# Kernel tuning notes

Hardware: AMD Instinct MI355X
Metric: run time of the kernel (lower is better)

Reference implementation:

```python
import jax, jax.numpy as jnp
import numpy as np

D_MODEL, D_STATE, D_CONV, D_INNER, DT_RANK = 1024, 16, 4, 2048, 64
B_SZ, L = 4, 2048

def setup_inputs() -> dict:
    key = jax.random.key(0)
    ks = jax.random.split(key, 7)
    return {
        "hidden_states": jax.random.normal(ks[0], (B_SZ, L, D_MODEL), jnp.float32),
        "in_proj_w": jax.random.normal(ks[1], (2 * D_INNER, D_MODEL), jnp.float32) * (D_MODEL ** -0.5),
        "conv_w": jax.random.normal(ks[2], (D_INNER, 1, D_CONV), jnp.float32) * 0.5,
        "conv_b": jax.random.normal(ks[3], (D_INNER,), jnp.float32) * 0.1,
        "x_proj_w": jax.random.normal(ks[4], (DT_RANK + 2 * D_STATE, D_INNER), jnp.float32) * (D_INNER ** -0.5),
        "dt_proj_w": jax.random.normal(ks[5], (D_INNER, DT_RANK), jnp.float32) * (DT_RANK ** -0.5),
        "A_log": jax.random.uniform(ks[6], (D_INNER, D_STATE), jnp.float32, 0.0, 2.0),
    }

def reference(hidden_states, in_proj_w, conv_w, conv_b, x_proj_w, dt_proj_w, A_log):
    b, l, d = hidden_states.shape
    # in_proj: (b,l,d) x (2*d_inner,d)^T -> (b, 2*d_inner, l)
    xz = jnp.einsum('bld,ed->bel', hidden_states, in_proj_w)
    x, z = jnp.split(xz, 2, axis=1)  # each (b, d_inner, l); z unused downstream
    A = -jnp.exp(A_log)              # (d_inner, d_state)
    # causal depthwise conv1d (left pad d_conv-1) + SiLU
    x = jax.lax.conv_general_dilated(
        x, conv_w, window_strides=(1,), padding=[(D_CONV - 1, 0)],
        feature_group_count=D_INNER,
        dimension_numbers=('NCH', 'OIH', 'NCH'))
    x = jax.nn.silu(x + conv_b[None, :, None])  # (b, d_inner, l)
    # x_proj: (b,l,dt_rank+2*d_state)
    x_dbl = jnp.einsum('bdl,ed->ble', x, x_proj_w)
    dt, B_mat, C_mat = jnp.split(x_dbl, [DT_RANK, DT_RANK + D_STATE], axis=-1)
    dt = jnp.einsum('blr,dr->bdl', dt, dt_proj_w)          # (b, d_inner, l), no bias
    B_mat = jnp.swapaxes(B_mat, 1, 2)                      # (b, d_state, l)
    C_mat = jnp.swapaxes(C_mat, 1, 2)                      # (b, d_state, l)
    return (dt, A, B_mat, C_mat, x)
```

## Files before the change

kernel.cpp:

```cpp
#include <hip/hip_runtime.h>
#include <hip/hip_bf16.h>
#include <math.h>

#define D_MODEL 1024
#define D_STATE 16
#define D_CONV  4
#define D_INNER 2048
#define DT_RANK 64
#define B_SZ    4
#define L_SEQ   2048

#define OFF_DT 0
#define OFF_A  (B_SZ * D_INNER * L_SEQ)
#define OFF_B  (OFF_A + D_INNER * D_STATE)
#define OFF_C  (OFF_B + B_SZ * D_STATE * L_SEQ)
#define OFF_X  (OFF_C + B_SZ * D_STATE * L_SEQ)

typedef __attribute__((ext_vector_type(8))) short bf16x8;
typedef __attribute__((ext_vector_type(8))) unsigned short us8;
typedef __attribute__((ext_vector_type(4))) float f32x4;
typedef unsigned short ushort_t;
typedef unsigned int uint_t;

static __device__ __forceinline__ ushort_t f2bf(float f) {
  __hip_bfloat16 h = __float2bfloat16(f);
  return *(ushort_t*)&h;
}
static __device__ __forceinline__ float bf2f(ushort_t u) {
  union { uint_t u; float f; } c;
  c.u = ((uint_t)u) << 16;
  return c.f;
}

#define N4_HS   (B_SZ * L_SEQ * D_MODEL / 4)
#define N4_W    (D_INNER * D_MODEL / 4)
#define N4_XW   ((DT_RANK + 2 * D_STATE) * D_INNER / 4)
#define N4_DW   (D_INNER * DT_RANK / 4)
#define N4_Z0   (B_SZ * DT_RANK * L_SEQ / 4)
#define N4_Z1   (2 * B_SZ * D_STATE * L_SEQ / 4)
#define N4_A    (D_INNER * D_STATE / 4)
#define N4_TOT  (N4_HS + N4_W + N4_XW + N4_DW + N4_Z0 + N4_Z1 + N4_A)

__global__ __launch_bounds__(256) void k_prep(
    const float4* __restrict__ hs, const float4* __restrict__ ipw,
    const float4* __restrict__ xpw, const float4* __restrict__ dpw,
    const float4* __restrict__ alog,
    ushort4* __restrict__ bfHS, ushort4* __restrict__ bfW,
    ushort4* __restrict__ xwb, ushort4* __restrict__ dwb,
    float4* __restrict__ z0, float4* __restrict__ z1,
    float4* __restrict__ aout) {
  int i = blockIdx.x * 256 + threadIdx.x;
  if (i < N4_HS) {
    float4 v = hs[i];
    ushort4 o; o.x = f2bf(v.x); o.y = f2bf(v.y); o.z = f2bf(v.z); o.w = f2bf(v.w);
    bfHS[i] = o;
    return;
  }
  i -= N4_HS;
  if (i < N4_W) {
    float4 v = ipw[i];
    ushort4 o; o.x = f2bf(v.x); o.y = f2bf(v.y); o.z = f2bf(v.z); o.w = f2bf(v.w);
    bfW[i] = o;
    return;
  }
  i -= N4_W;
  if (i < N4_XW) {
    float4 v = xpw[i];
    ushort4 o; o.x = f2bf(v.x); o.y = f2bf(v.y); o.z = f2bf(v.z); o.w = f2bf(v.w);
    xwb[i] = o;
    return;
  }
  i -= N4_XW;
  if (i < N4_DW) {
    float4 v = dpw[i];
    ushort4 o; o.x = f2bf(v.x); o.y = f2bf(v.y); o.z = f2bf(v.z); o.w = f2bf(v.w);
    dwb[i] = o;
    return;
  }
  i -= N4_DW;
  if (i < N4_Z0) { z0[i] = (float4){0.f, 0.f, 0.f, 0.f}; return; }
  i -= N4_Z0;
  if (i < N4_Z1) { z1[i] = (float4){0.f, 0.f, 0.f, 0.f}; return; }
  i -= N4_Z1;
  if (i < N4_A) {
    float4 v = alog[i];
    float4 o;
    o.x = -expf(v.x); o.y = -expf(v.y); o.z = -expf(v.z); o.w = -expf(v.w);
    aout[i] = o;
  }
}

__global__ __launch_bounds__(256) void k_inproj_mfma(
    const ushort_t* __restrict__ Wb,
    const ushort_t* __restrict__ HSb,
    ushort_t* __restrict__ Cout) {
  const int flat = blockIdx.x + 16 * blockIdx.y + 256 * blockIdx.z;
  const int swz  = (flat & 7) * 128 + (flat >> 3);
  const int bn = swz & 15;
  const int bm = (swz >> 4) & 15;
  const int b  = swz >> 8;

  __shared__ ushort_t As[2][128 * 32];
  __shared__ ushort_t Bs[2][128 * 32];
  const int tid  = threadIdx.x;
  const int wv   = tid >> 6;
  const int lane = tid & 63;
  const int wr = wv >> 1, wc = wv & 1;

  const int srow = tid >> 2;
  const int ss   = tid & 3;

  const ushort_t* Ag = Wb + (size_t)(bm * 128) * D_MODEL;
  const ushort_t* Bg = HSb + (size_t)b * L_SEQ * D_MODEL
                           + (size_t)(bn * 128) * D_MODEL;

  f32x4 acc[4][4];
#pragma unroll
  for (int i = 0; i < 4; ++i)
#pragma unroll
    for (int j = 0; j < 4; ++j) acc[i][j] = (f32x4){0.f, 0.f, 0.f, 0.f};

  const int ksel = lane >> 4;
  const int frow = lane & 15;

#define STAGE_IN(BUF, K0)                                                        \
  do {                                                                           \
    _Pragma("unroll")                                                            \
    for (int q = 0; q < 2; ++q) {                                                \
      int row = q * 64 + srow;                                                   \
      int xs  = ss ^ ((row >> 1) & 3);                                           \
      const ushort_t* ga = Ag + (size_t)row * D_MODEL + (K0) + xs * 8;           \
      const ushort_t* gb = Bg + (size_t)row * D_MODEL + (K0) + xs * 8;           \
      ushort_t* la = As[BUF] + (q * 256 + wv * 64) * 8;                          \
      ushort_t* lb = Bs[BUF] + (q * 256 + wv * 64) * 8;                          \
      __builtin_amdgcn_global_load_lds((const __attribute__((address_space(1))) void*)ga, \
                                       (__attribute__((address_space(3))) void*)la, 16, 0, 0); \
      __builtin_amdgcn_global_load_lds((const __attribute__((address_space(1))) void*)gb, \
                                       (__attribute__((address_space(3))) void*)lb, 16, 0, 0); \
    }                                                                            \
  } while (0)

  STAGE_IN(0, 0);
  __syncthreads();

  const int NT = D_MODEL / 32;
  for (int t = 0; t < NT; ++t) {
    const int cur = t & 1;
    if (t + 1 < NT) STAGE_IN(cur ^ 1, (t + 1) * 32);

    bf16x8 af[4], bfr[4];
#pragma unroll
    for (int m = 0; m < 4; ++m) {
      int row = wr * 64 + m * 16 + frow;
      af[m] = *(const bf16x8*)(As[cur] + (row * 4 + (ksel ^ ((row >> 1) & 3))) * 8);
    }
#pragma unroll
    for (int n = 0; n < 4; ++n) {
      int row = wc * 64 + n * 16 + frow;
      bfr[n] = *(const bf16x8*)(Bs[cur] + (row * 4 + (ksel ^ ((row >> 1) & 3))) * 8);
    }
#pragma unroll
    for (int m = 0; m < 4; ++m)
#pragma unroll
      for (int n = 0; n < 4; ++n)
        acc[m][n] = __builtin_amdgcn_mfma_f32_16x16x32_bf16(af[m], bfr[n], acc[m][n], 0, 0, 0);

    __syncthreads();
  }
#undef STAGE_IN

  const int crow0 = (lane >> 4) * 4;
  const int ccol  = lane & 15;
  ushort_t* Cb = Cout + (size_t)b * D_INNER * L_SEQ;
#pragma unroll
  for (int m = 0; m < 4; ++m) {
    int gr0 = bm * 128 + wr * 64 + m * 16 + crow0;
#pragma unroll
    for (int n = 0; n < 4; ++n) {
      int gc = bn * 128 + wc * 64 + n * 16 + ccol;
#pragma unroll
      for (int i = 0; i < 4; ++i)
        Cb[(size_t)(gr0 + i) * L_SEQ + gc] = f2bf(acc[m][n][i]);
    }
  }
}

__global__ __launch_bounds__(256) void k_xproj_fused(
    const ushort_t* __restrict__ XWb,
    const ushort_t* __restrict__ Xpre,
    const float* __restrict__ CW,
    const float* __restrict__ CB,
    float* __restrict__ Xout,
    float* __restrict__ XDBL,
    float* __restrict__ OutB,
    float* __restrict__ OutC) {
  const int ln = blockIdx.x;
  const int sk = blockIdx.y;
  const int b  = blockIdx.z;
  __shared__ ushort_t As[96 * 40];
  __shared__ ushort_t Bs[128 * 34];
  const int tid  = threadIdx.x;
  const int wv   = tid >> 6;
  const int lane = tid & 63;
  const int wr = wv >> 1, wc = wv & 1;
  const int ksel = lane >> 4;
  const int frow = lane & 15;

  f32x4 acc[3][4];
#pragma unroll
  for (int i = 0; i < 3; ++i)
#pragma unroll
    for (int j = 0; j < 4; ++j) acc[i][j] = (f32x4){0.f, 0.f, 0.f, 0.f};

  for (int k0 = 0; k0 < 256; k0 += 32) {
    const int koff = sk * 256 + k0;
    {
      int row = tid >> 2, s = tid & 3;
      bf16x8 v = *(const bf16x8*)(XWb + (size_t)row * D_INNER + koff + s * 8);
      *(bf16x8*)(As + row * 40 + s * 8) = v;
      if (tid < 128) {
        int row2 = 64 + (tid >> 2);
        bf16x8 v2 = *(const bf16x8*)(XWb + (size_t)row2 * D_INNER + koff + s * 8);
        *(bf16x8*)(As + row2 * 40 + s * 8) = v2;
      }
    }
#pragma unroll
    for (int j = 0; j < 2; ++j) {
      int u = tid + 256 * j;
      int n4 = u & 31;
      int kp = u >> 5;
      int l0 = ln * 128 + 4 * n4;
      float sv[2][4];
#pragma unroll
      for (int r = 0; r < 2; ++r) {
        int d = koff + 2 * kp + r;
        const ushort_t* row = Xpre + ((size_t)b * D_INNER + d) * L_SEQ;
        ushort4 cur = *(const ushort4*)(row + l0);
        float em3 = 0.f, em2 = 0.f, em1 = 0.f;
        if (l0 >= 4) {
          ushort4 pv = *(const ushort4*)(row + l0 - 4);
          em3 = bf2f(pv.y); em2 = bf2f(pv.z); em1 = bf2f(pv.w);
        }
        float ee[7] = {em3, em2, em1, bf2f(cur.x), bf2f(cur.y), bf2f(cur.z), bf2f(cur.w)};
        float4 w = *(const float4*)(CW + d * 4);
        float bias = CB[d];
#pragma unroll
        for (int i = 0; i < 4; ++i) {
          float v = w.x * ee[i] + w.y * ee[i + 1] + w.z * ee[i + 2] + w.w * ee[i + 3] + bias;
          sv[r][i] = v / (1.f + expf(-v));
        }
        *(float4*)(Xout + ((size_t)b * D_INNER + d) * L_SEQ + l0) =
            make_float4(sv[r][0], sv[r][1], sv[r][2], sv[r][3]);
      }
#pragma unroll
      for (int i = 0; i < 4; ++i) {
        uint_t pk = (uint_t)f2bf(sv[0][i]) | ((uint_t)f2bf(sv[1][i]) << 16);
        *(uint_t*)(Bs + (4 * n4 + i) * 34 + 2 * kp) = pk;
      }
    }
    __syncthreads();

    bf16x8 af[3], bfr[4];
#pragma unroll
    for (int mi = 0; mi < 3; ++mi) {
      int row = wr * 48 + mi * 16 + frow;
      af[mi] = *(const bf16x8*)(As + row * 40 + ksel * 8);
    }
#pragma unroll
    for (int ni = 0; ni < 4; ++ni) {
      int n = wc * 64 + ni * 16 + frow;
      const uint_t* p = (const uint_t*)(Bs + n * 34);
      union { uint_t u[4]; bf16x8 v; } fr;
#pragma unroll
      for (int q = 0; q < 4; ++q) fr.u[q] = p[ksel * 4 + q];
      bfr[ni] = fr.v;
    }
#pragma unroll
    for (int mi = 0; mi < 3; ++mi)
#pragma unroll
      for (int ni = 0; ni < 4; ++ni)
        acc[mi][ni] = __builtin_amdgcn_mfma_f32_16x16x32_bf16(af[mi], bfr[ni], acc[mi][ni], 0, 0, 0);
    __syncthreads();
  }

  const int crow0 = (lane >> 4) * 4;
  const int ccol  = lane & 15;
#pragma unroll
  for (int mi = 0; mi < 3; ++mi) {
    int e0 = wr * 48 + mi * 16 + crow0;
    float* base;
    int eoff;
    if (e0 < 64)      { base = XDBL + (size_t)b * 64 * L_SEQ; eoff = e0; }
    else if (e0 < 80) { base = OutB + (size_t)b * D_STATE * L_SEQ; eoff = e0 - 64; }
    else              { base = OutC + (size_t)b * D_STATE * L_SEQ; eoff = e0 - 80; }
#pragma unroll
    for (int ni = 0; ni < 4; ++ni) {
      int l = ln * 128 + wc * 64 + ni * 16 + ccol;
#pragma unroll
      for (int r = 0; r < 4; ++r)
        atomicAdd(base + (size_t)(eoff + r) * L_SEQ + l, acc[mi][ni][r]);
    }
  }
}

__global__ __launch_bounds__(256) void k_dt_mfma(
    const ushort_t* __restrict__ DWb,
    const float* __restrict__ XDBL,
    float* __restrict__ DT) {
  const int ln = blockIdx.x;
  const int dm = blockIdx.y;
  const int b  = blockIdx.z;
  __shared__ ushort_t As[128 * 72];
  __shared__ ushort_t Bs[128 * 68];
  const int tid  = threadIdx.x;
  const int wv   = tid >> 6;
  const int lane = tid & 63;
  const int wr = wv >> 1, wc = wv & 1;
  const int ksel = lane >> 4;
  const int frow = lane & 15;

#pragma unroll
  for (int q = 0; q < 4; ++q) {
    int u = tid + 256 * q;
    int row = u >> 3, s = u & 7;
    *(bf16x8*)(As + row * 72 + s * 8) =
        *(const bf16x8*)(DWb + (size_t)(dm * 128 + row) * DT_RANK + s * 8);
  }
#pragma unroll
  for (int q = 0; q < 4; ++q) {
    int u = tid + 256 * q;
    int n4 = u & 31;
    int kp = u >> 5;
    const float* g = XDBL + ((size_t)b * DT_RANK + 2 * kp) * L_SEQ + ln * 128 + 4 * n4;
    float4 x0 = *(const float4*)g;
    float4 x1 = *(const float4*)(g + L_SEQ);
    float e0[4] = {x0.x, x0.y, x0.z, x0.w};
    float e1[4] = {x1.x, x1.y, x1.z, x1.w};
#pragma unroll
    for (int i = 0; i < 4; ++i) {
      uint_t pk = (uint_t)f2bf(e0[i]) | ((uint_t)f2bf(e1[i]) << 16);
      *(uint_t*)(Bs + (4 * n4 + i) * 68 + 2 * kp) = pk;
    }
  }
  __syncthreads();

  f32x4 acc[4][4];
#pragma unroll
  for (int i = 0; i < 4; ++i)
#pragma unroll
    for (int j = 0; j < 4; ++j) acc[i][j] = (f32x4){0.f, 0.f, 0.f, 0.f};

#pragma unroll
  for (int ks = 0; ks < 2; ++ks) {
    bf16x8 af[4], bfr[4];
#pragma unroll
    for (int m = 0; m < 4; ++m) {
      int row = wr * 64 + m * 16 + frow;
      af[m] = *(const bf16x8*)(As + row * 72 + ks * 32 + ksel * 8);
    }
#pragma unroll
    for (int n = 0; n < 4; ++n) {
      int nn = wc * 64 + n * 16 + frow;
      bfr[n] = *(const bf16x8*)(Bs + nn * 68 + ks * 32 + ksel * 8);
    }
#pragma unroll
    for (int m = 0; m < 4; ++m)
#pragma unroll
      for (int n = 0; n < 4; ++n)
        acc[m][n] = __builtin_amdgcn_mfma_f32_16x16x32_bf16(af[m], bfr[n], acc[m][n], 0, 0, 0);
  }

  const int crow0 = (lane >> 4) * 4;
  const int ccol  = lane & 15;
  float* Cb = DT + (size_t)b * D_INNER * L_SEQ;
#pragma unroll
  for (int m = 0; m < 4; ++m) {
    int gr0 = dm * 128 + wr * 64 + m * 16 + crow0;
#pragma unroll
    for (int n = 0; n < 4; ++n) {
      int gc = ln * 128 + wc * 64 + n * 16 + ccol;
#pragma unroll
      for (int i = 0; i < 4; ++i)
        Cb[(size_t)(gr0 + i) * L_SEQ + gc] = acc[m][n][i];
    }
  }
}

extern "C" void kernel_launch(void* const* d_in, const int* in_sizes, int n_in,
                              void* d_out, int out_size, void* d_ws, size_t ws_size,
                              hipStream_t stream) {
  const float* hs   = (const float*)d_in[0];
  const float* ipw  = (const float*)d_in[1];
  const float* cw   = (const float*)d_in[2];
  const float* cb   = (const float*)d_in[3];
  const float* xpw  = (const float*)d_in[4];
  const float* dpw  = (const float*)d_in[5];
  const float* alog = (const float*)d_in[6];

  float* out    = (float*)d_out;
  float* dt_out = out + OFF_DT;
  float* a_out  = out + OFF_A;
  float* b_out  = out + OFF_B;
  float* c_out  = out + OFF_C;
  float* x_out  = out + OFF_X;

  unsigned short* bfHS = (unsigned short*)x_out;
  unsigned short* bfW  = bfHS + (size_t)B_SZ * L_SEQ * D_MODEL;
  unsigned short* xpre = (unsigned short*)dt_out;
  float* xdbl = (float*)d_ws;
  unsigned short* xwb = (unsigned short*)((char*)d_ws + 2097152);
  unsigned short* dwb = (unsigned short*)((char*)d_ws + 2097152 + 393216);

  k_prep<<<dim3((N4_TOT + 255) / 256), 256, 0, stream>>>(
      (const float4*)hs, (const float4*)ipw, (const float4*)xpw,
      (const float4*)dpw, (const float4*)alog,
      (ushort4*)bfHS, (ushort4*)bfW, (ushort4*)xwb, (ushort4*)dwb,
      (float4*)xdbl, (float4*)b_out, (float4*)a_out);

  k_inproj_mfma<<<dim3(16, 16, 4), 256, 0, stream>>>(bfW, bfHS, xpre);
  k_xproj_fused<<<dim3(16, 8, 4), 256, 0, stream>>>(xwb, xpre, cw, cb,
                                                    x_out, xdbl, b_out, c_out);
  k_dt_mfma<<<dim3(16, 16, 4), 256, 0, stream>>>(dwb, xdbl, dt_out);
}
```

Baseline: 134.6 us.

## Deepen in_proj GEMM prefetch pipeline and stage epilogue through LDS

The in_proj MFMA GEMM now keeps two K-tiles in flight. It waits with explicit vmcnt counters and raw s_barrier instead of __syncthreads each iteration, so global-to-LDS loads overlap more compute. The epilogue writes the bf16 tile into a padded shared buffer and then stores 16-byte vectors row by row, replacing the scattered 2-byte global stores. This relies on hand-counted vmcnt values and sched_barriers being correct, and it reuses the K-loop LDS for the output tile.

```diff
diff --git a/kernel.cpp b/kernel.cpp
--- a/kernel.cpp
+++ b/kernel.cpp
@@ -100,8 +100,7 @@
   const int bm = (swz >> 4) & 15;
   const int b  = swz >> 8;
 
-  __shared__ ushort_t As[2][128 * 32];
-  __shared__ ushort_t Bs[2][128 * 32];
+  __shared__ ushort_t sh[128 * 136];
   const int tid  = threadIdx.x;
   const int wv   = tid >> 6;
   const int lane = tid & 63;
@@ -131,8 +130,8 @@
       int xs  = ss ^ ((row >> 1) & 3);                                           \
       const ushort_t* ga = Ag + (size_t)row * D_MODEL + (K0) + xs * 8;           \
       const ushort_t* gb = Bg + (size_t)row * D_MODEL + (K0) + xs * 8;           \
-      ushort_t* la = As[BUF] + (q * 256 + wv * 64) * 8;                          \
-      ushort_t* lb = Bs[BUF] + (q * 256 + wv * 64) * 8;                          \
+      ushort_t* la = sh + (BUF) * 8192 + (q * 256 + wv * 64) * 8;                \
+      ushort_t* lb = sh + (BUF) * 8192 + 4096 + (q * 256 + wv * 64) * 8;         \
       __builtin_amdgcn_global_load_lds((const __attribute__((address_space(1))) void*)ga, \
                                        (__attribute__((address_space(3))) void*)la, 16, 0, 0); \
       __builtin_amdgcn_global_load_lds((const __attribute__((address_space(1))) void*)gb, \
@@ -140,48 +139,76 @@
     }                                                                            \
   } while (0)
 
+#define COMPUTE(BUF)                                                             \
+  do {                                                                           \
+    const ushort_t* Ab = sh + (BUF) * 8192;                                      \
+    const ushort_t* Bb = sh + (BUF) * 8192 + 4096;                               \
+    bf16x8 af[4], bfr[4];                                                        \
+    _Pragma("unroll")                                                            \
+    for (int m = 0; m < 4; ++m) {                                                \
+      int row = wr * 64 + m * 16 + frow;                                         \
+      af[m] = *(const bf16x8*)(Ab + (row * 4 + (ksel ^ ((row >> 1) & 3))) * 8);  \
+    }                                                                            \
+    _Pragma("unroll")                                                            \
+    for (int n = 0; n < 4; ++n) {                                                \
+      int row = wc * 64 + n * 16 + frow;                                         \
+      bfr[n] = *(const bf16x8*)(Bb + (row * 4 + (ksel ^ ((row >> 1) & 3))) * 8); \
+    }                                                                            \
+    _Pragma("unroll")                                                            \
+    for (int m = 0; m < 4; ++m)                                                  \
+      _Pragma("unroll")                                                          \
+      for (int n = 0; n < 4; ++n)                                                \
+        acc[m][n] = __builtin_amdgcn_mfma_f32_16x16x32_bf16(af[m], bfr[n], acc[m][n], 0, 0, 0); \
+  } while (0)
+
   STAGE_IN(0, 0);
+  STAGE_IN(1, 32);
+  asm volatile("s_waitcnt vmcnt(4)" ::: "memory");
+  __builtin_amdgcn_s_barrier();
+
+  for (int t = 0; t < 30; ++t) {
+    COMPUTE(t & 1);
+    __builtin_amdgcn_sched_barrier(0);
+    __builtin_amdgcn_s_barrier();
+    STAGE_IN(t & 1, (t + 2) * 32);
+    asm volatile("s_waitcnt vmcnt(4)" ::: "memory");
+    __builtin_amdgcn_s_barrier();
+    __builtin_amdgcn_sched_barrier(0);
+  }
+  COMPUTE(0);
+  __builtin_amdgcn_sched_barrier(0);
+  __builtin_amdgcn_s_barrier();
+  asm volatile("s_waitcnt vmcnt(0)" ::: "memory");
+  __builtin_amdgcn_s_barrier();
+  COMPUTE(1);
+#undef STAGE_IN
+#undef COMPUTE
+
   __syncthreads();
-
-  const int NT = D_MODEL / 32;
-  for (int t = 0; t < NT; ++t) {
-    const int cur = t & 1;
-    if (t + 1 < NT) STAGE_IN(cur ^ 1, (t + 1) * 32);
-
-    bf16x8 af[4], bfr[4];
-#pragma unroll
-    for (int m = 0; m < 4; ++m) {
-      int row = wr * 64 + m * 16 + frow;
-      af[m] = *(const bf16x8*)(As[cur] + (row * 4 + (ksel ^ ((row >> 1) & 3))) * 8);
-    }
-#pragma unroll
-    for (int n = 0; n < 4; ++n) {
-      int row = wc * 64 + n * 16 + frow;
-      bfr[n] = *(const bf16x8*)(Bs[cur] + (row * 4 + (ksel ^ ((row >> 1) & 3))) * 8);
-    }
-#pragma unroll
-    for (int m = 0; m < 4; ++m)
-#pragma unroll
-      for (int n = 0; n < 4; ++n)
-        acc[m][n] = __builtin_amdgcn_mfma_f32_16x16x32_bf16(af[m], bfr[n], acc[m][n], 0, 0, 0);
-
-    __syncthreads();
-  }
-#undef STAGE_IN
 
   const int crow0 = (lane >> 4) * 4;
   const int ccol  = lane & 15;
-  ushort_t* Cb = Cout + (size_t)b * D_INNER * L_SEQ;
 #pragma unroll
   for (int m = 0; m < 4; ++m) {
-    int gr0 = bm * 128 + wr * 64 + m * 16 + crow0;
 #pragma unroll
     for (int n = 0; n < 4; ++n) {
-      int gc = bn * 128 + wc * 64 + n * 16 + ccol;
+      int r0 = wr * 64 + m * 16 + crow0;
+      int c  = wc * 64 + n * 16 + ccol;
 #pragma unroll
       for (int i = 0; i < 4; ++i)
-        Cb[(size_t)(gr0 + i) * L_SEQ + gc] = f2bf(acc[m][n][i]);
-    }
+        sh[(r0 + i) * 136 + c] = f2bf(acc[m][n][i]);
+    }
+  }
+  __syncthreads();
+  ushort_t* Cb = Cout + (size_t)b * D_INNER * L_SEQ
+                      + (size_t)(bm * 128) * L_SEQ + bn * 128;
+#pragma unroll
+  for (int q = 0; q < 8; ++q) {
+    int idx = q * 256 + tid;
+    int r   = idx >> 4;
+    int c16 = idx & 15;
+    us8 v = *(const us8*)(sh + r * 136 + c16 * 8);
+    *(us8*)(Cb + (size_t)r * L_SEQ + c16 * 8) = v;
   }
 }
 
```

Result: faster. 129.7 us (-3.6%).
